# Performance work log

Measured on AMD Instinct MI355X. Metric: run time of the kernel, lower is better.

## Reference

```python
import jax, jax.numpy as jnp
import numpy as np

N = 100_000      # nodes
E = 1_600_000    # edges (before self loops)
F_IN = 128       # dataset.num_node_features
H = 64           # hidden_channels
C = 10           # dataset.num_classes
B = 128          # graphs in batch
NEG_SLOPE = 0.2  # GATConv default


def setup_inputs() -> dict:
    key = jax.random.key(0)
    ks = jax.random.split(key, 16)
    s = 0.05
    x = jax.random.normal(ks[0], (N, F_IN), jnp.float32)
    edge_index = jax.random.randint(ks[1], (2, E), 0, N, dtype=jnp.int32).astype(jnp.int64)
    batch = jnp.sort(jax.random.randint(ks[2], (N,), 0, B, dtype=jnp.int32)).astype(jnp.int64)
    inp = {"x": x, "edge_index": edge_index, "batch": batch}
    # GATConv params: lin weight [out,in], att_src/att_dst [out], bias [out]
    dims = [(H, F_IN), (H, H), (H, H)]
    for i, (o, fi) in enumerate(dims, start=1):
        k = jax.random.split(ks[2 + i], 4)
        inp[f"W{i}"] = jax.random.normal(k[0], (o, fi), jnp.float32) * s
        inp[f"a_src{i}"] = jax.random.normal(k[1], (o,), jnp.float32) * s
        inp[f"a_dst{i}"] = jax.random.normal(k[2], (o,), jnp.float32) * s
        inp[f"b{i}"] = jax.random.normal(k[3], (o,), jnp.float32) * s
    inp["W_lin"] = jax.random.normal(ks[8], (C, H), jnp.float32) * s
    inp["b_lin"] = jax.random.normal(ks[9], (C,), jnp.float32) * s
    return inp


def gat_conv(x, src, dst, W, a_src, a_dst, b):
    # x: [N,Fin]; src/dst: [E+N] (self loops appended)
    h = x @ W.T                      # [N,H]
    e_src = h @ a_src                # [N] per-node src score
    e_dst = h @ a_dst                # [N] per-node dst score
    e = jax.nn.leaky_relu(e_src[src] + e_dst[dst], NEG_SLOPE)  # [E+N]
    # segment softmax over incoming edges of each dst node
    m = jax.ops.segment_max(e, dst, num_segments=N)
    ex = jnp.exp(e - m[dst])
    denom = jax.ops.segment_sum(ex, dst, num_segments=N)
    alpha = ex / denom[dst]          # [E+N]
    out = jax.ops.segment_sum(h[src] * alpha[:, None], dst, num_segments=N)
    return out + b


def reference(x, edge_index, batch, W1, a_src1, a_dst1, b1,
              W2, a_src2, a_dst2, b2, W3, a_src3, a_dst3, b3,
              W_lin, b_lin):
    loops = jnp.arange(N, dtype=edge_index.dtype)
    src = jnp.concatenate([edge_index[0], loops])
    dst = jnp.concatenate([edge_index[1], loops])
    h = jax.nn.relu(gat_conv(x, src, dst, W1, a_src1, a_dst1, b1))
    h = jax.nn.relu(gat_conv(h, src, dst, W2, a_src2, a_dst2, b2))
    h = gat_conv(h, src, dst, W3, a_src3, a_dst3, b3)
    # global mean pool over graphs
    sums = jax.ops.segment_sum(h, batch, num_segments=B)          # [B,H]
    cnt = jax.ops.segment_sum(jnp.ones((N,), h.dtype), batch, num_segments=B)
    pooled = sums / jnp.maximum(cnt, 1.0)[:, None]
    # dropout is identity in eval mode
    return pooled @ W_lin.T + b_lin   # [B,C]
```

## Files before the change

### kernel.cpp

```cpp
#include <hip/hip_runtime.h>
#include <hip/hip_bf16.h>

#define NN 100000
#define EE 1600000
#define ETOT 1700000
#define FIN1 128
#define HD 64
#define NC 10
#define NB 128
#define NEG 0.2f
#define LOG2E 1.44269504f

#define NBKT 196
#define BCAP 10240
#define BLKE 2048
#define ABLOCKS ((ETOT + BLKE - 1) / BLKE)
#define GBLOCKS ((NN + 63) / 64)


static constexpr size_t OFF_HA   = 0;
static constexpr size_t OFF_HB   = (size_t)NN * HD;
static constexpr size_t OFF_ESA  = (size_t)NN * HD * 2;
static constexpr size_t OFF_EDA  = OFF_ESA + (size_t)NN * 4;
static constexpr size_t OFF_ESB  = OFF_EDA + (size_t)NN * 4;
static constexpr size_t OFF_EDB  = OFF_ESB + (size_t)NN * 4;
static constexpr size_t OFF_ROW  = OFF_EDB + (size_t)NN * 4;
static constexpr size_t OFF_CSR  = OFF_ROW + (size_t)(NN + 4) * 4;
static constexpr size_t OFF_GC   = OFF_CSR + (size_t)ETOT * 4;
static constexpr size_t OFF_POOL = OFF_GC + 1024;
static constexpr size_t OFF_BKT  = OFF_POOL + (size_t)NB * HD * 4;

typedef __attribute__((ext_vector_type(8))) short short8;
typedef __attribute__((ext_vector_type(4))) float floatx4;
typedef __attribute__((ext_vector_type(2))) float floatx2;

__device__ __forceinline__ unsigned short f2bf(float f) {
  unsigned u = __float_as_uint(f);
  if ((u & 0x7F800000u) == 0x7F800000u) return (unsigned short)(u >> 16);
  return (unsigned short)((u + 0x7FFFu + ((u >> 16) & 1u)) >> 16);
}
__device__ __forceinline__ unsigned pk2(float a, float b) {
  return (unsigned)f2bf(a) | ((unsigned)f2bf(b) << 16);
}

#if __has_builtin(__builtin_amdgcn_cvt_pk_fp8_f32) && __has_builtin(__builtin_amdgcn_cvt_pk_f32_fp8)
#define HW_FP8 1
#endif
__device__ __forceinline__ unsigned enc1_fp8(float f) {
  _Float16 hf = (_Float16)f;
  unsigned short b = __builtin_bit_cast(unsigned short, hf);
  unsigned s = ((unsigned)b >> 8) & 0x80u;
  int mag = b & 0x7fff;
  if (mag < 0x2380) return s;
  int r = mag + 0x3F + ((mag >> 7) & 1);
  int m = (r >> 7) - 64;
  if (m > 0x7E) m = 0x7E;
  return s | (unsigned)m;
}
__device__ __forceinline__ unsigned pack4_fp8(float a, float b, float c, float d) {
#ifdef HW_FP8
  int w = __builtin_amdgcn_cvt_pk_fp8_f32(a, b, 0, false);
  w = __builtin_amdgcn_cvt_pk_fp8_f32(c, d, w, true);
  return (unsigned)w;
#else
  return enc1_fp8(a) | (enc1_fp8(b) << 8) | (enc1_fp8(c) << 16) | (enc1_fp8(d) << 24);
#endif
}
__device__ __forceinline__ float dec1_fp8(unsigned byte) {
  unsigned short hb = (unsigned short)(((byte & 0x80u) << 8) | ((byte & 0x7fu) << 7));
  _Float16 hf = __builtin_bit_cast(_Float16, hb);
  return (float)hf * 256.0f;
}
template <bool HI>
__device__ __forceinline__ floatx2 unpk2_fp8(unsigned w) {
#ifdef HW_FP8
  return __builtin_amdgcn_cvt_pk_f32_fp8((int)w, HI);
#else
  unsigned s = HI ? (w >> 16) : w;
  floatx2 r; r.x = dec1_fp8(s & 0xffu); r.y = dec1_fp8((s >> 8) & 0xffu);
  return r;
#endif
}

__device__ __forceinline__ void bucketA_body(
    int bid, const int* __restrict__ EI, unsigned* __restrict__ bucketed,
    int* __restrict__ gcur, char* smem) {
  int* cnt = (int*)smem;
  int* base = cnt + NBKT;
  const int t = threadIdx.x;
  const long long start = (long long)bid * BLKE;
  unsigned pk[BLKE / 256];
  short bk[BLKE / 256];
  for (int i = t; i < NBKT; i += 256) cnt[i] = 0;
  __syncthreads();
#pragma unroll
  for (int j = 0; j < BLKE / 256; j++) {
    long long k = start + t + 256 * j;
    bk[j] = -1;
    if (k < ETOT) {
      int s, d;
      if (k < EE) { s = EI[k]; d = EI[(long long)EE + k]; }
      else        { s = d = (int)(k - EE); }
      int b = d >> 9;
      pk[j] = ((unsigned)s << 9) | (unsigned)(d & 511);
      bk[j] = (short)b;
      atomicAdd(&cnt[b], 1);
    }
  }
  __syncthreads();
  if (t < NBKT) {
    base[t] = (cnt[t] > 0) ? atomicAdd(&gcur[t], cnt[t]) : 0;
    cnt[t] = 0;
  }
  __syncthreads();
#pragma unroll
  for (int j = 0; j < BLKE / 256; j++) {
    if (bk[j] >= 0) {
      int b = bk[j];
      int pos = base[b] + atomicAdd(&cnt[b], 1);
      if (pos < BCAP) bucketed[(long long)b * BCAP + pos] = pk[j];
    }
  }
}

__device__ __forceinline__ void gemm1_body(
    int bid, const float* __restrict__ X, const float* __restrict__ W,
    const float* __restrict__ As, const float* __restrict__ Ad,
    unsigned* __restrict__ hout, float* __restrict__ es, float* __restrict__ ed,
    char* smem) {
  constexpr int K = FIN1, RW = K / 2;
  unsigned* Xw = (unsigned*)smem;
  unsigned* Ww = (unsigned*)(smem + 16384);
  const int t = threadIdx.x;
  const int nodeBase = bid * 64;

  for (int i4 = t * 4; i4 < 64 * K; i4 += 1024) {
    int node = i4 >> 7, k = i4 & (K - 1);
    float4 v = make_float4(0.f, 0.f, 0.f, 0.f);
    if (nodeBase + node < NN)
      v = *(const float4*)(X + ((long long)(nodeBase + node) << 7) + k);
    uint2 p = make_uint2(pk2(v.x, v.y), pk2(v.z, v.w));
    int kw = k >> 1;
    *(uint2*)&Xw[node * RW + (kw ^ ((node & 7) << 2))] = p;
  }
  for (int i4 = t * 4; i4 < 64 * K; i4 += 1024) {
    int f = i4 >> 7, k = i4 & (K - 1);
    float4 v = *(const float4*)(W + ((long long)f << 7) + k);
    uint2 p = make_uint2(pk2(v.x, v.y), pk2(v.z, v.w));
    int kw = k >> 1;
    *(uint2*)&Ww[f * RW + (kw ^ ((f & 7) << 2))] = p;
  }
  __syncthreads();

  const int w = t >> 6, l = t & 63, m = l & 15, q = l >> 4;
  const int nodeLoc = 16 * w + m;
  const int sxa = (nodeLoc & 7) << 2;
  floatx4 acc[4];
#pragma unroll
  for (int nt = 0; nt < 4; nt++) acc[nt] = (floatx4){0.f, 0.f, 0.f, 0.f};
#pragma unroll
  for (int kc = 0; kc < K; kc += 32) {
    const int kcw = (kc >> 1) + 4 * q;
    short8 af = *(const short8*)&Xw[nodeLoc * RW + (kcw ^ sxa)];
#pragma unroll
    for (int nt = 0; nt < 4; nt++) {
      int f = 16 * nt + m;
      short8 bf = *(const short8*)&Ww[f * RW + (kcw ^ ((f & 7) << 2))];
      acc[nt] = __builtin_amdgcn_mfma_f32_16x16x32_bf16(af, bf, acc[nt], 0, 0, 0);
    }
  }
  float asv[4], adv[4];
#pragma unroll
  for (int nt = 0; nt < 4; nt++) { asv[nt] = As[16 * nt + m]; adv[nt] = Ad[16 * nt + m]; }
#pragma unroll
  for (int r = 0; r < 4; r++) {
    float ss = 0.f, sd2 = 0.f;
#pragma unroll
    for (int nt = 0; nt < 4; nt++) {
      ss = fmaf(acc[nt][r], asv[nt], ss);
      sd2 = fmaf(acc[nt][r], adv[nt], sd2);
    }
#pragma unroll
    for (int off = 1; off < 16; off <<= 1) {
      ss += __shfl_xor(ss, off);
      sd2 += __shfl_xor(sd2, off);
    }
    if (m == 0) {
      int gn = nodeBase + 16 * w + 4 * q + r;
      if (gn < NN) { es[gn] = ss * LOG2E; ed[gn] = sd2 * LOG2E; }
    }
  }
  {
    int gn = nodeBase + 16 * w + 4 * q;
#pragma unroll
    for (int nt = 0; nt < 4; nt++) {
#pragma unroll
      for (int r = 0; r < 4; r++) {
        float v = acc[nt][r];
        float p1 = __shfl_xor(v, 1);
        float p2 = __shfl_xor(v, 2);
        float p3 = __shfl_xor(v, 3);
        if ((m & 3) == 0 && (gn + r) < NN)
          hout[(gn + r) * 16 + 4 * nt + (m >> 2)] = pack4_fp8(v, p1, p2, p3);
      }
    }
  }
}

__global__ __launch_bounds__(256) void buildA_gemm1_kernel(
    const int* __restrict__ EI, unsigned* __restrict__ bucketed, int* __restrict__ gcur,
    const float* __restrict__ X, const float* __restrict__ W,
    const float* __restrict__ As, const float* __restrict__ Ad,
    unsigned* __restrict__ hout, float* __restrict__ es, float* __restrict__ ed) {
  __shared__ __align__(16) char smem[32768];
  if (blockIdx.x < ABLOCKS)
    bucketA_body(blockIdx.x, EI, bucketed, gcur, smem);
  else
    gemm1_body(blockIdx.x - ABLOCKS, X, W, As, Ad, hout, es, ed, smem);
}

__global__ __launch_bounds__(1024) void bucketB_kernel(
    const unsigned* __restrict__ bucketed, const int* __restrict__ gcur,
    int* __restrict__ rowptr, int* __restrict__ csr) {
  __shared__ int sc[256];
  __shared__ int hist[512];
  __shared__ int cur[512];
  __shared__ int ssum[256];
  const int t = threadIdx.x;
  const int b = blockIdx.x;
  if (t < 256) sc[t] = (t < NBKT) ? gcur[t] : 0;
  __syncthreads();
  for (int off = 1; off < 256; off <<= 1) {
    int add = (t >= off && t < 256) ? sc[t - off] : 0;
    __syncthreads();
    if (t < 256) sc[t] += add;
    __syncthreads();
  }
  const int cnt = gcur[b];
  const int base = sc[b] - cnt;
  if (b == 0 && t == 0) rowptr[NN] = ETOT;
  const unsigned* bp = bucketed + (long long)b * BCAP;
  if (t < 512) hist[t] = 0;
  __syncthreads();
  for (int i = t; i < cnt; i += 1024) atomicAdd(&hist[bp[i] & 511], 1);
  __syncthreads();
  int a0 = 0, a1 = 0, s = 0;
  if (t < 256) {
    a0 = hist[2 * t];
    a1 = hist[2 * t + 1];
    s = a0 + a1;
    ssum[t] = s;
  }
  __syncthreads();
  for (int off = 1; off < 256; off <<= 1) {
    int add = (t >= off && t < 256) ? ssum[t - off] : 0;
    __syncthreads();
    if (t < 256) ssum[t] += add;
    __syncthreads();
  }
  if (t < 256) {
    int ex = ssum[t] - s;
    cur[2 * t] = ex;
    cur[2 * t + 1] = ex + a0;
    int gn = b * 512 + 2 * t;
    if (gn < NN) rowptr[gn] = base + ex;
    if (gn + 1 < NN) rowptr[gn + 1] = base + ex + a0;
  }
  __syncthreads();
  for (int i = t; i < cnt; i += 1024) {
    unsigned e = bp[i];
    int pos = atomicAdd(&cur[e & 511], 1);
    csr[base + pos] = (int)(e >> 9);
  }
}

__global__ __launch_bounds__(256) void agg_gemm_kernel(
    const int* __restrict__ rowptr, const int* __restrict__ csr,
    const float* __restrict__ esIn, const float* __restrict__ edIn,
    const uint2* __restrict__ h8In, const float* __restrict__ biasA,
    const float* __restrict__ W, const float* __restrict__ As,
    const float* __restrict__ Ad,
    unsigned* __restrict__ hOut, float* __restrict__ esOut, float* __restrict__ edOut) {
  constexpr int K = HD, RW = K / 2;
  __shared__ unsigned Xw[64 * RW];
  __shared__ unsigned Ww[64 * RW];
  const int t = threadIdx.x;
  const int nodeBase = blockIdx.x * 64;

  for (int i4 = t * 4; i4 < 64 * K; i4 += 1024) {
    int f = i4 >> 6, k = i4 & (K - 1);
    float4 v = *(const float4*)(W + ((long long)f << 6) + k);
    uint2 p = make_uint2(pk2(v.x, v.y), pk2(v.z, v.w));
    int kw = k >> 1;
    *(uint2*)&Ww[f * RW + (kw ^ ((f & 7) << 2))] = p;
  }

  const int fl = t & 7;
#pragma unroll
  for (int half = 0; half < 2; half++) {
    const int nl = half * 32 + (t >> 3);
    const int n = nodeBase + nl;
    const int sxa = (nl & 7) << 2;
    const int kwb = (4 * fl) ^ sxa;
    if (n < NN) {
      const float edn = edIn[n];
      const int row = rowptr[n];
      const int end = rowptr[n + 1];
      const int endm1 = end - 1;
      float den = 0.f;
      float acc[8];
#pragma unroll
      for (int j = 0; j < 8; j++) acc[j] = 0.f;
      for (int i = row; i < end; i += 4) {
        int k1 = i + 1, k2 = i + 2, k3 = i + 3;
        k1 = (k1 < end) ? k1 : endm1;
        k2 = (k2 < end) ? k2 : endm1;
        k3 = (k3 < end) ? k3 : endm1;
        int s0 = csr[i], s1 = csr[k1], s2 = csr[k2], s3 = csr[k3];
        uint2 u0 = h8In[s0 * 8 + fl];
        uint2 u1 = h8In[s1 * 8 + fl];
        uint2 u2 = h8In[s2 * 8 + fl];
        uint2 u3 = h8In[s3 * 8 + fl];
        float e0 = esIn[s0] + edn, e1 = esIn[s1] + edn;
        float e2 = esIn[s2] + edn, e3 = esIn[s3] + edn;
        e0 = fmaxf(e0, NEG * e0);
        e1 = fmaxf(e1, NEG * e1);
        e2 = fmaxf(e2, NEG * e2);
        e3 = fmaxf(e3, NEG * e3);
        float w0 = exp2f(e0), w1 = exp2f(e1), w2 = exp2f(e2), w3 = exp2f(e3);
        w1 = (i + 1 < end) ? w1 : 0.f;
        w2 = (i + 2 < end) ? w2 : 0.f;
        w3 = (i + 3 < end) ? w3 : 0.f;
        den += (w0 + w1) + (w2 + w3);
#define ACC_E(w, u)                                            \
        { floatx2 fA = unpk2_fp8<false>((u).x);                \
          floatx2 fB = unpk2_fp8<true>((u).x);                 \
          floatx2 fC = unpk2_fp8<false>((u).y);                \
          floatx2 fD = unpk2_fp8<true>((u).y);                 \
          acc[0] = fmaf(w, fA.x, acc[0]); acc[1] = fmaf(w, fA.y, acc[1]); \
          acc[2] = fmaf(w, fB.x, acc[2]); acc[3] = fmaf(w, fB.y, acc[3]); \
          acc[4] = fmaf(w, fC.x, acc[4]); acc[5] = fmaf(w, fC.y, acc[5]); \
          acc[6] = fmaf(w, fD.x, acc[6]); acc[7] = fmaf(w, fD.y, acc[7]); }
        ACC_E(w0, u0) ACC_E(w1, u1) ACC_E(w2, u2) ACC_E(w3, u3)
#undef ACC_E
      }
      const float inv = 1.0f / den;
      float v[8];
#pragma unroll
      for (int j = 0; j < 8; j++)
        v[j] = fmaxf(acc[j] * inv + biasA[8 * fl + j], 0.f);
      *(uint2*)&Xw[nl * RW + kwb] = make_uint2(pk2(v[0], v[1]), pk2(v[2], v[3]));
      *(uint2*)&Xw[nl * RW + kwb + 2] = make_uint2(pk2(v[4], v[5]), pk2(v[6], v[7]));
    } else {
      *(uint2*)&Xw[nl * RW + kwb] = make_uint2(0u, 0u);
      *(uint2*)&Xw[nl * RW + kwb + 2] = make_uint2(0u, 0u);
    }
  }
  __syncthreads();

  const int w = t >> 6, l = t & 63, m = l & 15, q = l >> 4;
  const int nodeLoc = 16 * w + m;
  const int sxa = (nodeLoc & 7) << 2;
  floatx4 acc[4];
#pragma unroll
  for (int nt = 0; nt < 4; nt++) acc[nt] = (floatx4){0.f, 0.f, 0.f, 0.f};
#pragma unroll
  for (int kc = 0; kc < K; kc += 32) {
    const int kcw = (kc >> 1) + 4 * q;
    short8 af = *(const short8*)&Xw[nodeLoc * RW + (kcw ^ sxa)];
#pragma unroll
    for (int nt = 0; nt < 4; nt++) {
      int f = 16 * nt + m;
      short8 bf = *(const short8*)&Ww[f * RW + (kcw ^ ((f & 7) << 2))];
      acc[nt] = __builtin_amdgcn_mfma_f32_16x16x32_bf16(af, bf, acc[nt], 0, 0, 0);
    }
  }
  float asv[4], adv[4];
#pragma unroll
  for (int nt = 0; nt < 4; nt++) { asv[nt] = As[16 * nt + m]; adv[nt] = Ad[16 * nt + m]; }
#pragma unroll
  for (int r = 0; r < 4; r++) {
    float ss = 0.f, sd2 = 0.f;
#pragma unroll
    for (int nt = 0; nt < 4; nt++) {
      ss = fmaf(acc[nt][r], asv[nt], ss);
      sd2 = fmaf(acc[nt][r], adv[nt], sd2);
    }
#pragma unroll
    for (int off = 1; off < 16; off <<= 1) {
      ss += __shfl_xor(ss, off);
      sd2 += __shfl_xor(sd2, off);
    }
    if (m == 0) {
      int gn = nodeBase + 16 * w + 4 * q + r;
      if (gn < NN) { esOut[gn] = ss * LOG2E; edOut[gn] = sd2 * LOG2E; }
    }
  }
  {
    int gn = nodeBase + 16 * w + 4 * q;
#pragma unroll
    for (int nt = 0; nt < 4; nt++) {
#pragma unroll
      for (int r = 0; r < 4; r++) {
        float v = acc[nt][r];
        float p1 = __shfl_xor(v, 1);
        float p2 = __shfl_xor(v, 2);
        float p3 = __shfl_xor(v, 3);
        if ((m & 3) == 0 && (gn + r) < NN)
          hOut[(gn + r) * 16 + 4 * nt + (m >> 2)] = pack4_fp8(v, p1, p2, p3);
      }
    }
  }
}

__global__ __launch_bounds__(256) void agg3_pool_kernel(
    const int* __restrict__ rowptr, const int* __restrict__ csr,
    const float* __restrict__ esIn, const float* __restrict__ edIn,
    const uint2* __restrict__ h8In, const float* __restrict__ biasA,
    const int* __restrict__ batch, float* __restrict__ pooled) {
  __shared__ float P[32 * 66];
  __shared__ int gl[32];
  const int t = threadIdx.x;
  const int fl = t & 7;
  const int nl = t >> 3;
  const int n = blockIdx.x * 32 + nl;
  if (t < 32) gl[t] = batch[blockIdx.x * 32 + t];
  {
    const float edn = edIn[n];
    const int row = rowptr[n];
    const int end = rowptr[n + 1];
    const int endm1 = end - 1;
    float den = 0.f;
    float acc[8];
#pragma unroll
    for (int j = 0; j < 8; j++) acc[j] = 0.f;
    for (int i = row; i < end; i += 4) {
      int k1 = i + 1, k2 = i + 2, k3 = i + 3;
      k1 = (k1 < end) ? k1 : endm1;
      k2 = (k2 < end) ? k2 : endm1;
      k3 = (k3 < end) ? k3 : endm1;
      int s0 = csr[i], s1 = csr[k1], s2 = csr[k2], s3 = csr[k3];
      uint2 u0 = h8In[s0 * 8 + fl];
      uint2 u1 = h8In[s1 * 8 + fl];
      uint2 u2 = h8In[s2 * 8 + fl];
      uint2 u3 = h8In[s3 * 8 + fl];
      float e0 = esIn[s0] + edn, e1 = esIn[s1] + edn;
      float e2 = esIn[s2] + edn, e3 = esIn[s3] + edn;
      e0 = fmaxf(e0, NEG * e0);
      e1 = fmaxf(e1, NEG * e1);
      e2 = fmaxf(e2, NEG * e2);
      e3 = fmaxf(e3, NEG * e3);
      float w0 = exp2f(e0), w1 = exp2f(e1), w2 = exp2f(e2), w3 = exp2f(e3);
      w1 = (i + 1 < end) ? w1 : 0.f;
      w2 = (i + 2 < end) ? w2 : 0.f;
      w3 = (i + 3 < end) ? w3 : 0.f;
      den += (w0 + w1) + (w2 + w3);
#define ACC_E(w, u)                                            \
      { floatx2 fA = unpk2_fp8<false>((u).x);                  \
        floatx2 fB = unpk2_fp8<true>((u).x);                   \
        floatx2 fC = unpk2_fp8<false>((u).y);                  \
        floatx2 fD = unpk2_fp8<true>((u).y);                   \
        acc[0] = fmaf(w, fA.x, acc[0]); acc[1] = fmaf(w, fA.y, acc[1]); \
        acc[2] = fmaf(w, fB.x, acc[2]); acc[3] = fmaf(w, fB.y, acc[3]); \
        acc[4] = fmaf(w, fC.x, acc[4]); acc[5] = fmaf(w, fC.y, acc[5]); \
        acc[6] = fmaf(w, fD.x, acc[6]); acc[7] = fmaf(w, fD.y, acc[7]); }
      ACC_E(w0, u0) ACC_E(w1, u1) ACC_E(w2, u2) ACC_E(w3, u3)
#undef ACC_E
    }
    const float inv = 1.0f / den;
#pragma unroll
    for (int j = 0; j < 8; j++)
      P[nl * 66 + 8 * fl + j] = acc[j] * inv + biasA[8 * fl + j];
  }
  __syncthreads();
  if (t < HD) {
    const int f = t;
    float s = 0.f;
    int gcur = gl[0];
    for (int k = 0; k < 32; k++) {
      int g = gl[k];
      if (g != gcur) {
        atomicAdd(&pooled[gcur * HD + f], s);
        s = 0.f;
        gcur = g;
      }
      s += P[k * 66 + f];
    }
    atomicAdd(&pooled[gcur * HD + f], s);
  }
}

__device__ __forceinline__ int lower_bound_batch(const int* bt, int target) {
  int lo = 0, hi = NN;
  while (lo < hi) {
    int mid = (lo + hi) >> 1;
    if (bt[mid] < target) lo = mid + 1; else hi = mid;
  }
  return lo;
}

__global__ void final_kernel(
    const float* __restrict__ pooled, const int* __restrict__ batch,
    const float* __restrict__ Wlin, const float* __restrict__ blin,
    float* __restrict__ out) {
  int t = blockIdx.x * blockDim.x + threadIdx.x;
  if (t >= NB * NC) return;
  int b = t / NC, c = t - b * NC;
  int lo = lower_bound_batch(batch, b);
  int hi = lower_bound_batch(batch, b + 1);
  float inv = 1.0f / fmaxf((float)(hi - lo), 1.0f);
  float a = blin[c];
#pragma unroll 16
  for (int f = 0; f < HD; f++)
    a = fmaf(pooled[b * HD + f] * inv, Wlin[(long long)c * HD + f], a);
  out[t] = a;
}

extern "C" void kernel_launch(void* const* d_in, const int* in_sizes, int n_in,
                              void* d_out, int out_size, void* d_ws, size_t ws_size,
                              hipStream_t stream) {
  char* ws = (char*)d_ws;
  unsigned* hA       = (unsigned*)(ws + OFF_HA);
  unsigned* hB       = (unsigned*)(ws + OFF_HB);
  float*    esA      = (float*)(ws + OFF_ESA);
  float*    edA      = (float*)(ws + OFF_EDA);
  float*    esB      = (float*)(ws + OFF_ESB);
  float*    edB      = (float*)(ws + OFF_EDB);
  int*      rowptr   = (int*)(ws + OFF_ROW);
  int*      csr      = (int*)(ws + OFF_CSR);
  int*      gcur     = (int*)(ws + OFF_GC);
  float*    pooled   = (float*)(ws + OFF_POOL);
  unsigned* bucketed = (unsigned*)(ws + OFF_BKT);

  const float* X  = (const float*)d_in[0];
  const int*   EI = (const int*)d_in[1];
  const int*   BT = (const int*)d_in[2];
  const float* Wm[3] = {(const float*)d_in[3], (const float*)d_in[7], (const float*)d_in[11]};
  const float* As[3] = {(const float*)d_in[4], (const float*)d_in[8], (const float*)d_in[12]};
  const float* Ad[3] = {(const float*)d_in[5], (const float*)d_in[9], (const float*)d_in[13]};
  const float* Bb[3] = {(const float*)d_in[6], (const float*)d_in[10], (const float*)d_in[14]};
  const float* Wl = (const float*)d_in[15];
  const float* bl = (const float*)d_in[16];

  (void)hipMemsetAsync(gcur, 0, 1024 + (size_t)NB * HD * 4, stream);
  buildA_gemm1_kernel<<<ABLOCKS + GBLOCKS, 256, 0, stream>>>(
      EI, bucketed, gcur, X, Wm[0], As[0], Ad[0], hA, esA, edA);
  bucketB_kernel<<<NBKT, 1024, 0, stream>>>(bucketed, gcur, rowptr, csr);
  agg_gemm_kernel<<<GBLOCKS, 256, 0, stream>>>(
      rowptr, csr, esA, edA, (const uint2*)hA, Bb[0],
      Wm[1], As[1], Ad[1], hB, esB, edB);
  agg_gemm_kernel<<<GBLOCKS, 256, 0, stream>>>(
      rowptr, csr, esB, edB, (const uint2*)hB, Bb[1],
      Wm[2], As[2], Ad[2], hA, esA, edA);
  agg3_pool_kernel<<<NN / 32, 256, 0, stream>>>(
      rowptr, csr, esA, edA, (const uint2*)hA, Bb[2], BT, pooled);
  final_kernel<<<(NB * NC + 255) / 256, 256, 0, stream>>>(pooled, BT, Wl, bl, (float*)d_out);
}
```

Baseline: 298.5 us.

## Stage bucketed edges in shared memory for contiguous global writes

The edge bucketing pass now computes per-block bucket offsets with a prefix scan, stages packed edges in LDS sorted by bucket, and then writes them out in order so each bucket's run in global memory is stored contiguously. The block size also doubles, which lengthens those runs and halves the number of global atomic reservations. The goal is to replace scattered global stores with coalesced ones. In exchange it adds LDS traffic, a log-step scan with many barriers, and larger per-thread register arrays, which can reduce occupancy.

```diff
diff --git a/kernel.cpp b/kernel.cpp
--- a/kernel.cpp
+++ b/kernel.cpp
@@ -13,7 +13,7 @@
 
 #define NBKT 196
 #define BCAP 10240
-#define BLKE 2048
+#define BLKE 4096
 #define ABLOCKS ((ETOT + BLKE - 1) / BLKE)
 #define GBLOCKS ((NN + 63) / 64)
 
@@ -85,10 +85,16 @@
 __device__ __forceinline__ void bucketA_body(
     int bid, const int* __restrict__ EI, unsigned* __restrict__ bucketed,
     int* __restrict__ gcur, char* smem) {
-  int* cnt = (int*)smem;
-  int* base = cnt + NBKT;
+  unsigned* stage = (unsigned*)smem;
+  unsigned short* sb = (unsigned short*)(smem + BLKE * 4);
+  int* cnt  = (int*)(smem + BLKE * 4 + BLKE * 2);
+  int* lofs = cnt + NBKT;
+  int* base = lofs + NBKT;
+  int* sc   = base + NBKT;
   const int t = threadIdx.x;
   const long long start = (long long)bid * BLKE;
+  long long rem = (long long)ETOT - start;
+  const int V = (rem < BLKE) ? (int)rem : BLKE;
   unsigned pk[BLKE / 256];
   short bk[BLKE / 256];
   for (int i = t; i < NBKT; i += 256) cnt[i] = 0;
@@ -108,8 +114,18 @@
     }
   }
   __syncthreads();
+  int own = (t < NBKT) ? cnt[t] : 0;
+  sc[t] = own;
+  __syncthreads();
+  for (int off = 1; off < 256; off <<= 1) {
+    int add = (t >= off) ? sc[t - off] : 0;
+    __syncthreads();
+    sc[t] += add;
+    __syncthreads();
+  }
   if (t < NBKT) {
-    base[t] = (cnt[t] > 0) ? atomicAdd(&gcur[t], cnt[t]) : 0;
+    lofs[t] = sc[t] - own;
+    base[t] = (own > 0) ? atomicAdd(&gcur[t], own) : 0;
     cnt[t] = 0;
   }
   __syncthreads();
@@ -117,9 +133,16 @@
   for (int j = 0; j < BLKE / 256; j++) {
     if (bk[j] >= 0) {
       int b = bk[j];
-      int pos = base[b] + atomicAdd(&cnt[b], 1);
-      if (pos < BCAP) bucketed[(long long)b * BCAP + pos] = pk[j];
-    }
+      int p = lofs[b] + atomicAdd(&cnt[b], 1);
+      stage[p] = pk[j];
+      sb[p] = (unsigned short)b;
+    }
+  }
+  __syncthreads();
+  for (int i = t; i < V; i += 256) {
+    int b = sb[i];
+    int pos = base[b] + (i - lofs[b]);
+    if (pos < BCAP) bucketed[(long long)b * BCAP + pos] = stage[i];
   }
 }
 
```

Measured after the change: 284.8 us. 1.05x faster.
